# Performance work log

Hardware: AMD Instinct MI355X
Metric: run time of the kernel (lower is better)

## Reference

```python
import jax, jax.numpy as jnp
import numpy as np

WINDOW_SIZE = (4, 7, 7)  # (t, h, w); N = 4*7*7 = 196


def _relative_position_index(ws):
    t, h, w = ws
    coords = np.stack(np.meshgrid(np.arange(t), np.arange(h), np.arange(w), indexing='ij'))  # (3,t,h,w)
    cf = coords.reshape(3, -1)                      # (3, N)
    rc = (cf[:, :, None] - cf[:, None, :]).transpose(1, 2, 0).astype(np.int64)  # (N, N, 3)
    rc[..., 0] += t - 1
    rc[..., 1] += h - 1
    rc[..., 2] += w - 1
    rc[..., 0] *= (2 * h - 1) * (2 * w - 1)
    rc[..., 1] *= 2 * w - 1
    return rc.sum(-1)                               # (N, N) indices into bias table


def setup_inputs() -> dict:
    key = jax.random.key(0)
    ks = jax.random.split(key, 7)
    B, B_dim, N, C, H = 4, 64, 196, 512, 16
    hd = C // H
    B_ = B * B_dim
    n_bias = (2 * 4 - 1) * (2 * 7 - 1) * (2 * 7 - 1)  # 1183
    return {
        'x': jax.random.normal(ks[0], (B_, N, C), jnp.float32),
        'q_global': jax.random.normal(ks[1], (B, 1, H, N, hd), jnp.float32),
        'kv_w': jax.random.normal(ks[2], (2 * C, C), jnp.float32) * (C ** -0.5),
        'kv_b': jnp.zeros((2 * C,), jnp.float32),
        'proj_w': jax.random.normal(ks[3], (C, C), jnp.float32) * (C ** -0.5),
        'proj_b': jnp.zeros((C,), jnp.float32),
        'bias_table': jax.random.normal(ks[4], (n_bias, H), jnp.float32) * 0.02,
    }


def reference(x, q_global, kv_w, kv_b, proj_w, proj_b, bias_table):
    B_, N, C = x.shape
    B, _, H, _, hd = q_global.shape
    B_dim = B_ // B
    scale = hd ** -0.5

    # kv projection: (B_, N, 2C) -> k, v each (B_, H, N, hd)
    kv = (x @ kv_w.T + kv_b).reshape(B_, N, 2, H, hd).transpose(2, 0, 3, 1, 4)
    keys, values = kv[0], kv[1]

    # global queries repeated across windows: (B,1,H,N,hd) -> (B_, H, N, hd)
    q = jnp.broadcast_to(q_global, (B, B_dim, H, N, hd)).reshape(B_, H, N, hd)
    q = q * scale

    attn = jnp.einsum('bhnd,bhmd->bhnm', q, keys)  # (B_, H, N, N)

    # gathered relative position bias (static index table)
    rpi = jnp.asarray(_relative_position_index(WINDOW_SIZE))  # (N, N)
    bias = bias_table[rpi.reshape(-1)].reshape(N, N, H).transpose(2, 0, 1)  # (H, N, N)
    attn = jax.nn.softmax(attn + bias[None], axis=-1)

    out = jnp.einsum('bhnm,bhmd->bhnd', attn, values)  # (B_, H, N, hd)
    out = out.transpose(0, 2, 1, 3).reshape(B_, N, C)
    return out @ proj_w.T + proj_b
```

## Files before the change

### kernel.cpp

```cpp
#include <hip/hip_runtime.h>
#include <stdint.h>

typedef __attribute__((ext_vector_type(8))) short short8;
typedef __attribute__((ext_vector_type(4))) float f32x4;
typedef __attribute__((ext_vector_type(4))) unsigned short u16x4;

typedef unsigned short ushort_t;

__device__ __forceinline__ unsigned short f2bf(float f) {
    union { float f; uint32_t u; } c; c.f = f;
    uint32_t u = c.u;
    return (unsigned short)((u + 0x7FFFu + ((u >> 16) & 1u)) >> 16);
}

__device__ __forceinline__ f32x4 mfma16(short8 a, short8 b, f32x4 c) {
    return __builtin_amdgcn_mfma_f32_16x16x32_bf16(a, b, c, 0, 0, 0);
}


__global__ __launch_bounds__(256) void cvt_x_k(const float4* __restrict__ in,
                                               u16x4* __restrict__ out, int n4) {
    int i = blockIdx.x * 256 + threadIdx.x;
    if (i < n4) {
        float4 v = in[i];
        u16x4 o;
        o[0] = f2bf(v.x); o[1] = f2bf(v.y); o[2] = f2bf(v.z); o[3] = f2bf(v.w);
        out[i] = o;
    }
}

__global__ __launch_bounds__(256) void cvt_small_k(const float4* __restrict__ kvw,
                                                   const float4* __restrict__ pw,
                                                   const float4* __restrict__ qg,
                                                   u16x4* __restrict__ kvwb,
                                                   u16x4* __restrict__ pwb,
                                                   u16x4* __restrict__ qb) {
    const float qs = 0.17677669529663687f;
    int i = blockIdx.x * 256 + threadIdx.x;
    if (i < 131072) {
        float4 v = kvw[i];
        u16x4 o; o[0]=f2bf(v.x); o[1]=f2bf(v.y); o[2]=f2bf(v.z); o[3]=f2bf(v.w);
        kvwb[i] = o;
    } else if (i < 196608) {
        int j = i - 131072;
        float4 v = pw[j];
        u16x4 o; o[0]=f2bf(v.x); o[1]=f2bf(v.y); o[2]=f2bf(v.z); o[3]=f2bf(v.w);
        pwb[j] = o;
    } else {
        int j = i - 196608;
        float4 v = qg[j];
        u16x4 o; o[0]=f2bf(v.x*qs); o[1]=f2bf(v.y*qs); o[2]=f2bf(v.z*qs); o[3]=f2bf(v.w*qs);
        qb[j] = o;
    }
}

__global__ __launch_bounds__(256) void bias_k(const float* __restrict__ bt,
                                              float* __restrict__ out) {
    int idx = blockIdx.x * 256 + threadIdx.x;
    int h = idx / 43264;
    int rem = idx - h * 43264;
    int i = rem / 208;
    int j = rem - i * 208;
    float v = -1e30f;
    if (i < 196 && j < 196) {
        int t1 = i / 49, r1 = i - t1 * 49, h1 = r1 / 7, w1 = r1 - h1 * 7;
        int t2 = j / 49, r2 = j - t2 * 49, h2 = r2 / 7, w2 = r2 - h2 * 7;
        int bi = (t1 - t2 + 3) * 169 + (h1 - h2 + 6) * 13 + (w1 - w2 + 6);
        v = bt[bi * 16 + h];
    }
    out[idx] = v;
}

__global__ __launch_bounds__(256) void gemm_kv(const ushort_t* __restrict__ A,
                                               const ushort_t* __restrict__ Bw,
                                               const float* __restrict__ kvb,
                                               ushort_t* __restrict__ Ko,
                                               ushort_t* __restrict__ Vo) {
    __shared__ ushort_t As[128 * 72];
    __shared__ ushort_t Bs[128 * 72];
    const int tid = threadIdx.x;
    const int lane = tid & 63, wave = tid >> 6;
    const int lrow = lane & 15, quad = lane >> 4;
    const int wr = wave >> 1, wc = wave & 1;
    const long arow0 = (long)blockIdx.x * 128;
    const int brow0 = blockIdx.y * 128;

    f32x4 acc[4][4];
#pragma unroll
    for (int i = 0; i < 4; ++i)
#pragma unroll
        for (int j = 0; j < 4; ++j) acc[i][j] = (f32x4){0.f, 0.f, 0.f, 0.f};

    for (int k0 = 0; k0 < 512; k0 += 64) {
        short8 ar[4], br[4];
#pragma unroll
        for (int it = 0; it < 4; ++it) {
            int c = it * 256 + tid;
            int row = c >> 3, cc = c & 7;
            ar[it] = *(const short8*)&A[(arow0 + row) * 512 + k0 + cc * 8];
            br[it] = *(const short8*)&Bw[(long)(brow0 + row) * 512 + k0 + cc * 8];
        }
        __syncthreads();
#pragma unroll
        for (int it = 0; it < 4; ++it) {
            int c = it * 256 + tid;
            int row = c >> 3, cc = c & 7;
            *(short8*)&As[row * 72 + cc * 8] = ar[it];
            *(short8*)&Bs[row * 72 + cc * 8] = br[it];
        }
        __syncthreads();
#pragma unroll
        for (int kk = 0; kk < 64; kk += 32) {
            short8 af[4], bf[4];
#pragma unroll
            for (int i = 0; i < 4; ++i)
                af[i] = *(const short8*)&As[(wr * 64 + i * 16 + lrow) * 72 + kk + quad * 8];
#pragma unroll
            for (int j = 0; j < 4; ++j)
                bf[j] = *(const short8*)&Bs[(wc * 64 + j * 16 + lrow) * 72 + kk + quad * 8];
#pragma unroll
            for (int i = 0; i < 4; ++i)
#pragma unroll
                for (int j = 0; j < 4; ++j)
                    acc[i][j] = mfma16(af[i], bf[j], acc[i][j]);
        }
    }
#pragma unroll
    for (int i = 0; i < 4; ++i) {
        int mb = (int)arow0 + wr * 64 + i * 16 + quad * 4;
#pragma unroll
        for (int r = 0; r < 4; ++r) {
            int m = mb + r;
            int b_ = m / 196;
            int n = m - b_ * 196;
#pragma unroll
            for (int j = 0; j < 4; ++j) {
                int cI = brow0 + wc * 64 + j * 16 + lrow;
                float v = acc[i][j][r] + kvb[cI];
                int hh = (cI >> 5) & 15, d = cI & 31;
                ushort_t* dst = (cI >> 9) ? Vo : Ko;
                dst[((((long)b_ << 4) + hh) * 196 + n) * 32 + d] = f2bf(v);
            }
        }
    }
}

__global__ __launch_bounds__(256) void attn_k(const ushort_t* __restrict__ Kb,
                                              const ushort_t* __restrict__ Vb,
                                              const ushort_t* __restrict__ Qb,
                                              const float* __restrict__ biasF,
                                              ushort_t* __restrict__ Ob) {
    const int tid = threadIdx.x, lane = tid & 63, wave = tid >> 6;
    const int lrow = lane & 15, quad = lane >> 4;
    const int bh = blockIdx.x;
    const int b_ = bh >> 4, h = bh & 15;
    const int Bq = b_ >> 6;

    __shared__ ushort_t Ks[208 * 40];
    __shared__ ushort_t Vt[32 * 232];
    __shared__ ushort_t Ps[4][16 * 232];

    const long kvoff = (long)bh * 6272;

    for (int c = tid; c < 784; c += 256) {
        int n = c >> 2, dp = c & 3;
        *(short8*)&Ks[n * 40 + dp * 8] = *(const short8*)&Kb[kvoff + n * 32 + dp * 8];
    }
    for (int i = tid; i < 12 * 40; i += 256) Ks[196 * 40 + i] = 0;
    for (int i = tid; i < 6272; i += 256) {
        int n = i >> 5, d = i & 31;
        Vt[d * 232 + n] = Vb[kvoff + i];
    }
    for (int i = tid; i < 32 * 36; i += 256) {
        int d = i / 36, j = i - d * 36;
        Vt[d * 232 + 196 + j] = 0;
    }
    for (int i = lane; i < 256; i += 64) {
        int r = i >> 4, cp = i & 15;
        Ps[wave][r * 232 + 208 + cp] = 0;
    }
    __syncthreads();

    const float* biasH = biasF + h * 43264;
    const long qbase = (((long)Bq * 16 + h) * 196) * 32;

    for (int rt = wave; rt < 13; rt += 4) {
        int qrow = rt * 16 + lrow; if (qrow > 195) qrow = 195;
        short8 qf = *(const short8*)&Qb[qbase + (long)qrow * 32 + quad * 8];

        f32x4 s[13];
#pragma unroll
        for (int ct = 0; ct < 13; ++ct) {
            short8 kf = *(const short8*)&Ks[(ct * 16 + lrow) * 40 + quad * 8];
            s[ct] = mfma16(qf, kf, (f32x4){0.f, 0.f, 0.f, 0.f});
        }
        const int srow0 = rt * 16 + quad * 4;
        float mx[4], sm[4];
#pragma unroll
        for (int r = 0; r < 4; ++r) mx[r] = -3e38f;
#pragma unroll
        for (int ct = 0; ct < 13; ++ct) {
            const float* bp = biasH + (long)srow0 * 208 + ct * 16 + lrow;
#pragma unroll
            for (int r = 0; r < 4; ++r) {
                float v = s[ct][r] + bp[r * 208];
                s[ct][r] = v;
                mx[r] = fmaxf(mx[r], v);
            }
        }
#pragma unroll
        for (int r = 0; r < 4; ++r) {
            mx[r] = fmaxf(mx[r], __shfl_xor(mx[r], 1, 16));
            mx[r] = fmaxf(mx[r], __shfl_xor(mx[r], 2, 16));
            mx[r] = fmaxf(mx[r], __shfl_xor(mx[r], 4, 16));
            mx[r] = fmaxf(mx[r], __shfl_xor(mx[r], 8, 16));
            sm[r] = 0.f;
        }
#pragma unroll
        for (int ct = 0; ct < 13; ++ct)
#pragma unroll
            for (int r = 0; r < 4; ++r) {
                float p = __expf(s[ct][r] - mx[r]);
                s[ct][r] = p;
                sm[r] += p;
            }
#pragma unroll
        for (int r = 0; r < 4; ++r) {
            sm[r] += __shfl_xor(sm[r], 1, 16);
            sm[r] += __shfl_xor(sm[r], 2, 16);
            sm[r] += __shfl_xor(sm[r], 4, 16);
            sm[r] += __shfl_xor(sm[r], 8, 16);
            sm[r] = 1.0f / sm[r];
        }
        ushort_t* prow = &Ps[wave][0];
#pragma unroll
        for (int ct = 0; ct < 13; ++ct)
#pragma unroll
            for (int r = 0; r < 4; ++r)
                prow[(quad * 4 + r) * 232 + ct * 16 + lrow] = f2bf(s[ct][r] * sm[r]);
        asm volatile("s_waitcnt lgkmcnt(0)" ::: "memory");

        f32x4 o0 = (f32x4){0.f,0.f,0.f,0.f}, o1 = (f32x4){0.f,0.f,0.f,0.f};
#pragma unroll
        for (int ks = 0; ks < 7; ++ks) {
            short8 pf = *(const short8*)&prow[lrow * 232 + ks * 32 + quad * 8];
            short8 v0 = *(const short8*)&Vt[lrow * 232 + ks * 32 + quad * 8];
            short8 v1 = *(const short8*)&Vt[(16 + lrow) * 232 + ks * 32 + quad * 8];
            o0 = mfma16(pf, v0, o0);
            o1 = mfma16(pf, v1, o1);
        }
        const long obase = (long)b_ * 196 * 512 + h * 32;
#pragma unroll
        for (int r = 0; r < 4; ++r) {
            int m = srow0 + r;
            if (m < 196) {
                Ob[obase + (long)m * 512 + lrow]      = f2bf(o0[r]);
                Ob[obase + (long)m * 512 + 16 + lrow] = f2bf(o1[r]);
            }
        }
    }
}

__global__ __launch_bounds__(256) void gemm_proj(const ushort_t* __restrict__ A,
                                                 const ushort_t* __restrict__ Bw,
                                                 const float* __restrict__ pb,
                                                 float* __restrict__ out) {
    __shared__ ushort_t As[128 * 72];
    __shared__ ushort_t Bs[128 * 72];
    const int tid = threadIdx.x;
    const int lane = tid & 63, wave = tid >> 6;
    const int lrow = lane & 15, quad = lane >> 4;
    const int wr = wave >> 1, wc = wave & 1;
    const long arow0 = (long)blockIdx.x * 128;
    const int brow0 = blockIdx.y * 128;

    f32x4 acc[4][4];
#pragma unroll
    for (int i = 0; i < 4; ++i)
#pragma unroll
        for (int j = 0; j < 4; ++j) acc[i][j] = (f32x4){0.f, 0.f, 0.f, 0.f};

    for (int k0 = 0; k0 < 512; k0 += 64) {
        short8 ar[4], br[4];
#pragma unroll
        for (int it = 0; it < 4; ++it) {
            int c = it * 256 + tid;
            int row = c >> 3, cc = c & 7;
            ar[it] = *(const short8*)&A[(arow0 + row) * 512 + k0 + cc * 8];
            br[it] = *(const short8*)&Bw[(long)(brow0 + row) * 512 + k0 + cc * 8];
        }
        __syncthreads();
#pragma unroll
        for (int it = 0; it < 4; ++it) {
            int c = it * 256 + tid;
            int row = c >> 3, cc = c & 7;
            *(short8*)&As[row * 72 + cc * 8] = ar[it];
            *(short8*)&Bs[row * 72 + cc * 8] = br[it];
        }
        __syncthreads();
#pragma unroll
        for (int kk = 0; kk < 64; kk += 32) {
            short8 af[4], bf[4];
#pragma unroll
            for (int i = 0; i < 4; ++i)
                af[i] = *(const short8*)&As[(wr * 64 + i * 16 + lrow) * 72 + kk + quad * 8];
#pragma unroll
            for (int j = 0; j < 4; ++j)
                bf[j] = *(const short8*)&Bs[(wc * 64 + j * 16 + lrow) * 72 + kk + quad * 8];
#pragma unroll
            for (int i = 0; i < 4; ++i)
#pragma unroll
                for (int j = 0; j < 4; ++j)
                    acc[i][j] = mfma16(af[i], bf[j], acc[i][j]);
        }
    }
#pragma unroll
    for (int i = 0; i < 4; ++i) {
        long mb = arow0 + wr * 64 + i * 16 + quad * 4;
#pragma unroll
        for (int r = 0; r < 4; ++r) {
            long m = mb + r;
#pragma unroll
            for (int j = 0; j < 4; ++j) {
                int cI = brow0 + wc * 64 + j * 16 + lrow;
                out[m * 512 + cI] = acc[i][j][r] + pb[cI];
            }
        }
    }
}


extern "C" void kernel_launch(void* const* d_in, const int* in_sizes, int n_in,
                              void* d_out, int out_size, void* d_ws, size_t ws_size,
                              hipStream_t stream) {
    const float* x   = (const float*)d_in[0];
    const float* qg  = (const float*)d_in[1];
    const float* kvw = (const float*)d_in[2];
    const float* kvb = (const float*)d_in[3];
    const float* pw  = (const float*)d_in[4];
    const float* pb  = (const float*)d_in[5];
    const float* bt  = (const float*)d_in[6];
    float* out = (float*)d_out;

    char* ws = (char*)d_ws;
    ushort_t* xb    = (ushort_t*)(ws);
    ushort_t* kbuf  = (ushort_t*)(ws + 51380224);
    ushort_t* vbuf  = (ushort_t*)(ws + 102760448);
    ushort_t* kvwb  = (ushort_t*)(ws + 154140672);
    ushort_t* pwb   = (ushort_t*)(ws + 155189248);
    ushort_t* qb    = (ushort_t*)(ws + 155713536);
    float*    biasF = (float*)   (ws + 156516352);
    ushort_t* obuf  = xb;

    cvt_x_k<<<25088, 256, 0, stream>>>((const float4*)x, (u16x4*)xb, 6422528);
    cvt_small_k<<<1160, 256, 0, stream>>>((const float4*)kvw, (const float4*)pw,
                                          (const float4*)qg,
                                          (u16x4*)kvwb, (u16x4*)pwb, (u16x4*)qb);
    bias_k<<<2704, 256, 0, stream>>>(bt, biasF);
    gemm_kv<<<dim3(392, 8), 256, 0, stream>>>(xb, kvwb, kvb, kbuf, vbuf);
    attn_k<<<4096, 256, 0, stream>>>(kbuf, vbuf, qb, biasF, obuf);
    gemm_proj<<<dim3(392, 4), 256, 0, stream>>>(obuf, pwb, pb, out);
}
```

Before: 463.6 us.

## Restructure attention kernel: transposed QK, exp2 softmax, deferred normalization, 8 waves

The attention kernel now computes S^T (K as the A operand), so each lane holds four consecutive key columns of one query row. That allows float4 bias loads, two cross-lane shuffles instead of per-row 16-lane reductions, and packed bf16 conversion stores into LDS. K is read directly from global memory rather than staged in shared memory. Q and bias are prescaled by log2(e) so exp2f can be used, and the 1/sum normalization is applied to the output instead of to P. Blocks grow to 512 threads (8 waves, one row tile each), which changes occupancy and LDS use per block. The trade-off is unnormalized bf16 P, which may change rounding.

```diff
diff --git a/kernel.cpp b/kernel.cpp
--- a/kernel.cpp
+++ b/kernel.cpp
@@ -16,6 +16,8 @@
 __device__ __forceinline__ f32x4 mfma16(short8 a, short8 b, f32x4 c) {
     return __builtin_amdgcn_mfma_f32_16x16x32_bf16(a, b, c, 0, 0, 0);
 }
+
+#define LOG2E 1.4426950408889634f
 
 
 __global__ __launch_bounds__(256) void cvt_x_k(const float4* __restrict__ in,
@@ -35,7 +37,7 @@
                                                    u16x4* __restrict__ kvwb,
                                                    u16x4* __restrict__ pwb,
                                                    u16x4* __restrict__ qb) {
-    const float qs = 0.17677669529663687f;
+    const float qs = 0.17677669529663687f * LOG2E;
     int i = blockIdx.x * 256 + threadIdx.x;
     if (i < 131072) {
         float4 v = kvw[i];
@@ -66,7 +68,7 @@
         int t1 = i / 49, r1 = i - t1 * 49, h1 = r1 / 7, w1 = r1 - h1 * 7;
         int t2 = j / 49, r2 = j - t2 * 49, h2 = r2 / 7, w2 = r2 - h2 * 7;
         int bi = (t1 - t2 + 3) * 169 + (h1 - h2 + 6) * 13 + (w1 - w2 + 6);
-        v = bt[bi * 16 + h];
+        v = bt[bi * 16 + h] * LOG2E;
     }
     out[idx] = v;
 }
@@ -145,33 +147,27 @@
     }
 }
 
-__global__ __launch_bounds__(256) void attn_k(const ushort_t* __restrict__ Kb,
-                                              const ushort_t* __restrict__ Vb,
-                                              const ushort_t* __restrict__ Qb,
-                                              const float* __restrict__ biasF,
-                                              ushort_t* __restrict__ Ob) {
+__global__ __launch_bounds__(512, 4) void attn_k(const ushort_t* __restrict__ Kb,
+                                                 const ushort_t* __restrict__ Vb,
+                                                 const ushort_t* __restrict__ Qb,
+                                                 const float* __restrict__ biasF,
+                                                 ushort_t* __restrict__ Ob) {
     const int tid = threadIdx.x, lane = tid & 63, wave = tid >> 6;
     const int lrow = lane & 15, quad = lane >> 4;
     const int bh = blockIdx.x;
     const int b_ = bh >> 4, h = bh & 15;
     const int Bq = b_ >> 6;
 
-    __shared__ ushort_t Ks[208 * 40];
     __shared__ ushort_t Vt[32 * 232];
-    __shared__ ushort_t Ps[4][16 * 232];
+    __shared__ ushort_t Ps[8][16 * 232];
 
     const long kvoff = (long)bh * 6272;
 
-    for (int c = tid; c < 784; c += 256) {
-        int n = c >> 2, dp = c & 3;
-        *(short8*)&Ks[n * 40 + dp * 8] = *(const short8*)&Kb[kvoff + n * 32 + dp * 8];
-    }
-    for (int i = tid; i < 12 * 40; i += 256) Ks[196 * 40 + i] = 0;
-    for (int i = tid; i < 6272; i += 256) {
+    for (int i = tid; i < 6272; i += 512) {
         int n = i >> 5, d = i & 31;
         Vt[d * 232 + n] = Vb[kvoff + i];
     }
-    for (int i = tid; i < 32 * 36; i += 256) {
+    for (int i = tid; i < 32 * 36; i += 512) {
         int d = i / 36, j = i - d * 36;
         Vt[d * 232 + 196 + j] = 0;
     }
@@ -183,67 +179,59 @@
 
     const float* biasH = biasF + h * 43264;
     const long qbase = (((long)Bq * 16 + h) * 196) * 32;
-
-    for (int rt = wave; rt < 13; rt += 4) {
-        int qrow = rt * 16 + lrow; if (qrow > 195) qrow = 195;
-        short8 qf = *(const short8*)&Qb[qbase + (long)qrow * 32 + quad * 8];
+    const ushort_t* Kh = Kb + kvoff;
+
+    for (int rt = wave; rt < 13; rt += 8) {
+        const int qrow = rt * 16 + lrow;
+        const int qr = qrow > 195 ? 195 : qrow;
+        short8 qf = *(const short8*)&Qb[qbase + (long)qr * 32 + quad * 8];
 
         f32x4 s[13];
 #pragma unroll
         for (int ct = 0; ct < 13; ++ct) {
-            short8 kf = *(const short8*)&Ks[(ct * 16 + lrow) * 40 + quad * 8];
-            s[ct] = mfma16(qf, kf, (f32x4){0.f, 0.f, 0.f, 0.f});
-        }
-        const int srow0 = rt * 16 + quad * 4;
-        float mx[4], sm[4];
-#pragma unroll
-        for (int r = 0; r < 4; ++r) mx[r] = -3e38f;
+            short8 kf = *(const short8*)&Kh[(ct * 16 + lrow) * 32 + quad * 8];
+            s[ct] = mfma16(kf, qf, (f32x4){0.f, 0.f, 0.f, 0.f});
+        }
+
+        float mx = -3e38f;
+        const float* bp = biasH + (long)qrow * 208 + quad * 4;
 #pragma unroll
         for (int ct = 0; ct < 13; ++ct) {
-            const float* bp = biasH + (long)srow0 * 208 + ct * 16 + lrow;
+            float4 bv = *(const float4*)&bp[ct * 16];
+            s[ct][0] += bv.x; s[ct][1] += bv.y; s[ct][2] += bv.z; s[ct][3] += bv.w;
+            mx = fmaxf(mx, fmaxf(fmaxf(s[ct][0], s[ct][1]), fmaxf(s[ct][2], s[ct][3])));
+        }
+        mx = fmaxf(mx, __shfl_xor(mx, 16));
+        mx = fmaxf(mx, __shfl_xor(mx, 32));
+
+        float sm = 0.f;
+#pragma unroll
+        for (int ct = 0; ct < 13; ++ct)
 #pragma unroll
             for (int r = 0; r < 4; ++r) {
-                float v = s[ct][r] + bp[r * 208];
-                s[ct][r] = v;
-                mx[r] = fmaxf(mx[r], v);
+                float p = exp2f(s[ct][r] - mx);
+                s[ct][r] = p;
+                sm += p;
             }
-        }
-#pragma unroll
-        for (int r = 0; r < 4; ++r) {
-            mx[r] = fmaxf(mx[r], __shfl_xor(mx[r], 1, 16));
-            mx[r] = fmaxf(mx[r], __shfl_xor(mx[r], 2, 16));
-            mx[r] = fmaxf(mx[r], __shfl_xor(mx[r], 4, 16));
-            mx[r] = fmaxf(mx[r], __shfl_xor(mx[r], 8, 16));
-            sm[r] = 0.f;
-        }
-#pragma unroll
-        for (int ct = 0; ct < 13; ++ct)
-#pragma unroll
-            for (int r = 0; r < 4; ++r) {
-                float p = __expf(s[ct][r] - mx[r]);
-                s[ct][r] = p;
-                sm[r] += p;
-            }
-#pragma unroll
-        for (int r = 0; r < 4; ++r) {
-            sm[r] += __shfl_xor(sm[r], 1, 16);
-            sm[r] += __shfl_xor(sm[r], 2, 16);
-            sm[r] += __shfl_xor(sm[r], 4, 16);
-            sm[r] += __shfl_xor(sm[r], 8, 16);
-            sm[r] = 1.0f / sm[r];
-        }
-        ushort_t* prow = &Ps[wave][0];
-#pragma unroll
-        for (int ct = 0; ct < 13; ++ct)
-#pragma unroll
-            for (int r = 0; r < 4; ++r)
-                prow[(quad * 4 + r) * 232 + ct * 16 + lrow] = f2bf(s[ct][r] * sm[r]);
+        sm += __shfl_xor(sm, 16);
+        sm += __shfl_xor(sm, 32);
+        const float sminv = 1.0f / sm;
+
+        ushort_t* prow = &Ps[wave][lrow * 232];
+#pragma unroll
+        for (int ct = 0; ct < 13; ++ct) {
+            uint32_t w0, w1;
+            asm("v_cvt_pk_bf16_f32 %0, %1, %2" : "=v"(w0) : "v"(s[ct][0]), "v"(s[ct][1]));
+            asm("v_cvt_pk_bf16_f32 %0, %1, %2" : "=v"(w1) : "v"(s[ct][2]), "v"(s[ct][3]));
+            uint2 w; w.x = w0; w.y = w1;
+            *(uint2*)&prow[ct * 16 + quad * 4] = w;
+        }
         asm volatile("s_waitcnt lgkmcnt(0)" ::: "memory");
 
         f32x4 o0 = (f32x4){0.f,0.f,0.f,0.f}, o1 = (f32x4){0.f,0.f,0.f,0.f};
 #pragma unroll
         for (int ks = 0; ks < 7; ++ks) {
-            short8 pf = *(const short8*)&prow[lrow * 232 + ks * 32 + quad * 8];
+            short8 pf = *(const short8*)&prow[ks * 32 + quad * 8];
             short8 v0 = *(const short8*)&Vt[lrow * 232 + ks * 32 + quad * 8];
             short8 v1 = *(const short8*)&Vt[(16 + lrow) * 232 + ks * 32 + quad * 8];
             o0 = mfma16(pf, v0, o0);
@@ -252,10 +240,11 @@
         const long obase = (long)b_ * 196 * 512 + h * 32;
 #pragma unroll
         for (int r = 0; r < 4; ++r) {
-            int m = srow0 + r;
+            float sv = __shfl(sminv, quad * 4 + r);
+            int m = rt * 16 + quad * 4 + r;
             if (m < 196) {
-                Ob[obase + (long)m * 512 + lrow]      = f2bf(o0[r]);
-                Ob[obase + (long)m * 512 + 16 + lrow] = f2bf(o1[r]);
+                Ob[obase + (long)m * 512 + lrow]      = f2bf(o0[r] * sv);
+                Ob[obase + (long)m * 512 + 16 + lrow] = f2bf(o1[r] * sv);
             }
         }
     }
@@ -358,6 +347,6 @@
                                           (u16x4*)kvwb, (u16x4*)pwb, (u16x4*)qb);
     bias_k<<<2704, 256, 0, stream>>>(bt, biasF);
     gemm_kv<<<dim3(392, 8), 256, 0, stream>>>(xb, kvwb, kvb, kbuf, vbuf);
-    attn_k<<<4096, 256, 0, stream>>>(kbuf, vbuf, qb, biasF, obuf);
+    attn_k<<<4096, 512, 0, stream>>>(kbuf, vbuf, qb, biasF, obuf);
     gemm_proj<<<dim3(392, 4), 256, 0, stream>>>(obuf, pwb, pb, out);
 }
```

Result: slower. 493.5 us (+6.5%).
